# Kernel tuning notes

Measured on AMD Instinct MI355X. Metric: run time of the kernel, lower is better.

Reference implementation:

```python
import jax, jax.numpy as jnp
import numpy as np

ALPHA = 2000.0   # alpha (bandwidth penalty)
K = 8            # number of modes
MAX_N = 20       # max ADMM iterations; tol=0 -> loop always runs MAX_N-1 iters
DC = False


def setup_inputs() -> dict:
    key = jax.random.key(0)
    signal = jax.random.normal(key, (16, 8192), dtype=jnp.float32)  # (C, T)
    return {"signal": signal}


def _forward(signal):
    C, T = signal.shape
    F = 2 * T
    # mirror extension -> (C, 2T)
    f = jnp.concatenate([signal[:, :T // 2][:, ::-1], signal, signal[:, T // 2:][:, ::-1]], axis=1)
    t = jnp.linspace(1.0 / F, 1.0, F)
    freqs = (t - 0.5 - 1.0 / F).astype(jnp.float32)                  # (F,)
    # NOTE: torch.fft.fftshift with default dim shifts ALL dims (incl. channel dim);
    # jnp.fft.fftshift with axes=None matches this behavior exactly.
    f_hat = jnp.fft.fftshift(jnp.fft.fft(f))
    f_hat_plus = f_hat.at[:, :F // 2].set(0)                         # zero negative freqs
    fpos = f_hat_plus.T.astype(jnp.complex64)                        # (F, C)
    freqs_c = freqs.astype(jnp.complex64)
    fh = freqs[F // 2:]                                              # positive freqs (F/2,)
    alpha_c = jnp.complex64(ALPHA)

    omega0 = ((0.5 / K) * jnp.arange(K, dtype=jnp.float32)).astype(jnp.complex64)  # init == 1
    u0 = jnp.zeros((F, K, C), jnp.complex64)
    sum0 = jnp.zeros((F, C), jnp.complex64)

    def omega_update(u_k):                                           # u_k: (F, C)
        p = jnp.abs(u_k[F // 2:, :]) ** 2                            # (F/2, C)
        return (jnp.sum(fh @ p) / jnp.sum(p)).astype(jnp.complex64)

    def step(carry, _):
        u_prev, omega_prev, sum_uk = carry
        sum_uk = sum_uk + u_prev[:, K - 1, :] - u_prev[:, 0, :]
        us, omegas = [], []
        for k in range(K):                                           # sequential mode recurrence
            if k > 0:
                sum_uk = sum_uk + us[k - 1] - u_prev[:, k, :]
            # torch uses omega from the PREVIOUS outer iteration for all modes
            denom = 1.0 + alpha_c * jnp.square(freqs_c - omega_prev[k])   # (F,)
            u_k = (fpos - sum_uk) / denom[:, None]   # lamda_hat stays 0 (never updated in torch)
            us.append(u_k)
            if k == 0 and DC:
                omegas.append(jnp.complex64(0.0))
            else:
                omegas.append(omega_update(u_k))
        u_curr = jnp.stack(us, axis=1)                               # (F, K, C)
        omega_curr = jnp.stack(omegas)                               # (K,)
        return (u_curr, omega_curr, sum_uk), omega_curr

    (u_fin, _, _), omega_hist = jax.lax.scan(step, (u0, omega0, sum0), None, length=MAX_N - 1)
    omega = jnp.concatenate([omega0[None, :], omega_hist], axis=0)   # (MAX_N, K)

    # Hermitian completion of the half-spectrum (matches torch index assignments & order)
    pos = u_fin[F // 2:, :, :]                                       # (F/2, K, C)
    u_hat = jnp.zeros((F, K, C), jnp.complex64)
    u_hat = u_hat.at[F // 2:].set(pos)
    u_hat = u_hat.at[jnp.arange(F // 2, 0, -1)].set(jnp.conj(pos))   # overwrites bin F/2 w/ conj
    u_hat = u_hat.at[0].set(jnp.conj(u_hat[-1]))

    u_time = jnp.fft.ifft(jnp.fft.ifftshift(u_hat, axes=0), axis=0).real  # (F, K, C)
    u_c = jnp.transpose(u_time, (1, 0, 2)).astype(jnp.complex64)          # (K, F, C)
    u_c = u_c[:, F // 4:3 * F // 4, :]                                    # crop mirror -> (K, T, C)
    u_hat2 = jnp.conj(jnp.fft.fftshift(jnp.fft.fft(u_c, axis=1), axes=1)) # (K, T, C)
    u_hat2 = jnp.transpose(u_hat2, (1, 0, 2))                             # (T, K, C)
    # torch applies ifftshift with dim=-1, which is the CHANNEL dim here; replicate faithfully
    u_out = jnp.fft.ifftshift(u_c, axes=-1).real                          # (K, T, C)
    return u_out, u_hat2, omega


def reference(signal):
    return _forward(signal)
```

## Files before the change

### kernel.cpp

```cpp
#include <hip/hip_runtime.h>
#include <math.h>

#define NPAIR 131072
#define STEPS 19
#define VMD_BLOCKS 256
#define ND_BANKS 16

#define SW(a) ((a) ^ (((a) >> 5) & 31))

#define LD_RLX(p)    __hip_atomic_load((p),       __ATOMIC_RELAXED, __HIP_MEMORY_SCOPE_AGENT)
#define ST_RLX(p,v)  __hip_atomic_store((p),(v),  __ATOMIC_RELAXED, __HIP_MEMORY_SCOPE_AGENT)
#define FAA_RLX(p,v) __hip_atomic_fetch_add((p),(v),__ATOMIC_RELAXED, __HIP_MEMORY_SCOPE_AGENT)

#define D_NDB   0
#define D_CNT   4864
#define D_OHIST 5400

__device__ __forceinline__ float2 cadd(float2 a, float2 b){ return make_float2(a.x+b.x, a.y+b.y); }
__device__ __forceinline__ float2 csub(float2 a, float2 b){ return make_float2(a.x-b.x, a.y-b.y); }
__device__ __forceinline__ float2 cmul(float2 a, float2 b){
    return make_float2(a.x*b.x - a.y*b.y, a.x*b.y + a.y*b.x);
}
template<int SGN>
__device__ __forceinline__ float2 imul(float2 a){
    return (SGN > 0) ? make_float2(-a.y, a.x) : make_float2(a.y, -a.x);
}

template<int SGN>
__device__ __forceinline__ void dft8(const float2* a, float2* y){
    const float C = 0.70710678118654752f;
    const float sg = (SGN > 0) ? 1.f : -1.f;
    float2 t0 = cadd(a[0], a[4]), t1 = csub(a[0], a[4]);
    float2 t2 = cadd(a[2], a[6]), t3 = imul<SGN>(csub(a[2], a[6]));
    float2 E0 = cadd(t0, t2), E2 = csub(t0, t2), E1 = cadd(t1, t3), E3 = csub(t1, t3);
    float2 s0 = cadd(a[1], a[5]), s1 = csub(a[1], a[5]);
    float2 s2 = cadd(a[3], a[7]), s3 = imul<SGN>(csub(a[3], a[7]));
    float2 O0 = cadd(s0, s2), O2 = csub(s0, s2), O1 = cadd(s1, s3), O3 = csub(s1, s3);
    float2 w1 = make_float2(C, sg * C), w3 = make_float2(-C, sg * C);
    float2 R0 = O0, R1 = cmul(O1, w1), R2 = imul<SGN>(O2), R3 = cmul(O3, w3);
    y[0] = cadd(E0, R0); y[4] = csub(E0, R0);
    y[1] = cadd(E1, R1); y[5] = csub(E1, R1);
    y[2] = cadd(E2, R2); y[6] = csub(E2, R2);
    y[3] = cadd(E3, R3); y[7] = csub(E3, R3);
}

template<int SGN>
__device__ void lds_fft8192_r8(float2* lds, int tid){
    #pragma unroll
    for (int pi = 0; pi < 4; pi++){
        int ls = 3 * pi;
        int s  = 1 << ls;
        int nn = 8192 >> ls;
        int q = tid & (s - 1);
        float2 a[8], y[8];
        #pragma unroll
        for (int r = 0; r < 8; r++) a[r] = lds[SW(tid + (r << 10))];
        __syncthreads();
        dft8<SGN>(a, y);
        int p = tid >> ls;
        float ang = (float)(2 * p) / (float)nn;
        float sn, cs;
        sincospif(SGN > 0 ? ang : -ang, &sn, &cs);
        float2 w = make_float2(cs, sn);
        float2 wk = make_float2(1.f, 0.f);
        int o = q + ((tid - q) << 3);
        lds[SW(o)] = y[0];
        #pragma unroll
        for (int k = 1; k < 8; k++){
            wk = cmul(wk, w);
            lds[SW(o + (k << ls))] = cmul(y[k], wk);
        }
        __syncthreads();
    }
    #pragma unroll
    for (int w4 = 0; w4 < 4; w4++){
        int idx = (w4 << 10) + tid;
        float2 a = lds[SW(idx)], b = lds[SW(idx + 4096)];
        lds[SW(idx)]        = cadd(a, b);
        lds[SW(idx + 4096)] = csub(a, b);
    }
    __syncthreads();
}

template<int SGN>
__device__ void lds_fft4096_r8(float2* lds, int tid){
    #pragma unroll
    for (int pi = 0; pi < 4; pi++){
        int ls = 3 * pi;
        int s  = 1 << ls;
        int nn = 4096 >> ls;
        float2 a[8], y[8];
        int q = tid & (s - 1);
        if (tid < 512){
            #pragma unroll
            for (int r = 0; r < 8; r++) a[r] = lds[SW(tid + (r << 9))];
        }
        __syncthreads();
        if (tid < 512){
            dft8<SGN>(a, y);
            int p = tid >> ls;
            float ang = (float)(2 * p) / (float)nn;
            float sn, cs;
            sincospif(SGN > 0 ? ang : -ang, &sn, &cs);
            float2 w = make_float2(cs, sn);
            float2 wk = make_float2(1.f, 0.f);
            int o = q + ((tid - q) << 3);
            lds[SW(o)] = y[0];
            #pragma unroll
            for (int k = 1; k < 8; k++){
                wk = cmul(wk, w);
                lds[SW(o + (k << ls))] = cmul(y[k], wk);
            }
        }
        __syncthreads();
    }
}

__global__ __launch_bounds__(512) void k_stageA(const float* __restrict__ sig,
                                                float2* __restrict__ C,
                                                double* __restrict__ D){
    extern __shared__ float2 lds[];
    int tid = threadIdx.x;
    int bb  = blockIdx.x;
    int zi = bb * 512 + tid;
    if (zi < 5400) D[zi] = 0.0;
    int cw = bb >> 2, r4 = bb & 3;
    int cs = (cw + 8) & 15;
    const float* sp = sig + cs * 8192;
    #pragma unroll
    for (int i = 0; i < 8; i++){
        int p = i * 512 + tid;
        int x = 4 * p + r4;
        int mx = (x < 4096) ? (4095 - x) : ((x < 12288) ? (x - 4096) : (20479 - x));
        lds[SW(p)] = make_float2(sp[mx], 0.f);
    }
    __syncthreads();
    lds_fft4096_r8<-1>(lds, tid);
    float2* dst = C + (size_t)bb * 4096;
    #pragma unroll
    for (int i = 0; i < 8; i++){
        int j = i * 512 + tid;
        dst[j] = lds[SW(j)];
    }
}

__global__ __launch_bounds__(512, 2) void k_vmd_all(const float2* __restrict__ C,
                                                    float2* __restrict__ U,
                                                    double* __restrict__ D){
    double* NDB   = D + D_NDB;
    int*    CNT   = (int*)(D + D_CNT);
    double* OHIST = D + D_OHIST;

    int tid = blockIdx.x * 512 + threadIdx.x;
    int j = tid & 8191;
    int cw = tid >> 13;
    float fr = (float)j / 16384.0f;
    const float2* Cb = C + (size_t)(cw * 4) * 4096;
    int m = j & 4095;
    float2 C0 = Cb[m], C1 = Cb[4096 + m], C2 = Cb[8192 + m], C3 = Cb[12288 + m];
    float s1, c1, s2, c2;
    sincospif(-(float)j / 8192.0f, &s1, &c1);
    sincospif(-(float)j / 4096.0f, &s2, &c2);
    float2 w1 = make_float2(c1, s1), w2 = make_float2(c2, s2), w3 = cmul(w1, w2);
    float2 fv = cadd(cadd(C0, cmul(w1, C1)), cadd(cmul(w2, C2), cmul(w3, C3)));
    float fx = fv.x, fy = fv.y;
    float urx[8], ury[8], om[8];
    #pragma unroll
    for (int k = 0; k < 8; k++){ urx[k] = 0.f; ury[k] = 0.f; om[k] = 0.0625f * (float)k; }
    __shared__ float  lred[8][16];
    __shared__ double om_s[8];
    int lane = threadIdx.x & 63, wv = threadIdx.x >> 6;
    int mybank = (blockIdx.x & (ND_BANKS - 1)) * 16;
    int grp = blockIdx.x >> 4;

    for (int step = 0; step < STEPS; step++){
        if (step > 0){
            #pragma unroll
            for (int k = 0; k < 8; k++) om[k] = (float)om_s[k];
        }
        float sx = 0.f, sy = 0.f;
        #pragma unroll
        for (int k = 1; k < 8; k++){ sx += urx[k]; sy += ury[k]; }
        float lx = 0.f, ly = 0.f, nloc[8], dloc[8];
        #pragma unroll
        for (int k = 0; k < 8; k++){
            if (k > 0){ sx += lx - urx[k]; sy += ly - ury[k]; }
            float d = fr - om[k];
            float den = 1.0f + 2000.0f * d * d;
            float rden = 1.0f / den;
            float nx = (fx - sx) * rden, ny = (fy - sy) * rden;
            urx[k] = nx; ury[k] = ny;
            lx = nx; ly = ny;
            float pw = nx * nx + ny * ny;
            nloc[k] = fr * pw; dloc[k] = pw;
        }
        float s8[8];
        {
            bool hi = (lane & 32) != 0;
            #pragma unroll
            for (int k = 0; k < 8; k++){
                float t = hi ? nloc[k] : dloc[k];
                float r = __shfl_xor(t, 32);
                s8[k] = (hi ? dloc[k] : nloc[k]) + r;
            }
        }
        float s4v[4];
        {
            bool hi = (lane & 16) != 0;
            #pragma unroll
            for (int k = 0; k < 4; k++){
                float t = hi ? s8[k] : s8[k + 4];
                float r = __shfl_xor(t, 16);
                s4v[k] = (hi ? s8[k + 4] : s8[k]) + r;
            }
        }
        float s2v[2];
        {
            bool hi = (lane & 8) != 0;
            #pragma unroll
            for (int k = 0; k < 2; k++){
                float t = hi ? s4v[k] : s4v[k + 2];
                float r = __shfl_xor(t, 8);
                s2v[k] = (hi ? s4v[k + 2] : s4v[k]) + r;
            }
        }
        float sv;
        {
            bool hi = (lane & 4) != 0;
            float t = hi ? s2v[0] : s2v[1];
            float r = __shfl_xor(t, 4);
            sv = (hi ? s2v[1] : s2v[0]) + r;
        }
        sv += __shfl_xor(sv, 2);
        sv += __shfl_xor(sv, 1);
        if ((lane & 3) == 0) lred[wv][lane >> 2] = sv;
        __syncthreads();
        if (threadIdx.x < 16){
            double sum = 0.0;
            #pragma unroll
            for (int w = 0; w < 8; w++) sum += (double)lred[w][threadIdx.x];
            atomicAdd(&NDB[step * 256 + mybank + threadIdx.x], sum);
        }
        __syncthreads();
        if (step < STEPS - 1){
            if (threadIdx.x == 0){
                int target = 16 * (step + 1);
                int old = FAA_RLX(&CNT[grp * 32], 1);
                bool released = false;
                if (old == target - 1){
                    int rold = FAA_RLX(&CNT[512], 1);
                    if (rold == target - 1){
                        #pragma unroll
                        for (int g = 0; g < 16; g++)
                            ST_RLX(&CNT[576 + g * 32], step + 1);
                        released = true;
                    }
                }
                if (!released)
                    while (LD_RLX(&CNT[576 + grp * 32]) <= step) { }
            }
            __syncthreads();
            if (threadIdx.x < 8){
                const double* row = &NDB[step * 256];
                double n_ = 0.0, d_ = 0.0;
                #pragma unroll
                for (int bk = 0; bk < ND_BANKS; bk++){
                    n_ += LD_RLX(&row[bk * 16 + threadIdx.x]);
                    d_ += LD_RLX(&row[bk * 16 + 8 + threadIdx.x]);
                }
                double v = n_ / d_;
                om_s[threadIdx.x] = v;
                if (blockIdx.x == 0)
                    ST_RLX(&OHIST[step * 8 + threadIdx.x], v);
            }
            __syncthreads();
        }
    }
    #pragma unroll
    for (int k = 0; k < 8; k++) U[k * NPAIR + tid] = make_float2(urx[k], ury[k]);
}

__global__ __launch_bounds__(1024) void k_stageCD(float2* __restrict__ U){
    extern __shared__ float2 lds[];
    int tid = threadIdx.x;
    int b = blockIdx.x;
    const float2* pos = U + b * 8192;
    float* slice = (float*)(U) + (size_t)b * 16384;
    const float inv = 1.0f / 16384.0f;
    #pragma unroll
    for (int r = 0; r < 8; r++){
        int p = r * 1024 + tid;
        float2 Hk, HkM;
        if (p == 0){
            Hk  = make_float2(pos[0].x, 0.f);
            HkM = make_float2(pos[8191].x, 0.f);
        } else {
            Hk = pos[p];
            float2 q2 = pos[8192 - p];
            HkM = make_float2(q2.x, -q2.y);
        }
        float2 S  = cadd(Hk, HkM);
        float2 Dv = csub(Hk, HkM);
        float sn, cn;
        sincospif((float)p / 8192.0f, &sn, &cn);
        float2 c = cmul(make_float2(cn, sn), Dv);
        lds[SW(p)] = make_float2(S.x - c.y, S.y + c.x);
    }
    __syncthreads();
    lds_fft8192_r8<1>(lds, tid);
    float2 zreg[4];
    #pragma unroll
    for (int q = 2; q < 6; q++){
        int n = q * 1024 + tid;
        float2 z = lds[SW(n)];
        zreg[q - 2] = make_float2(z.x * inv, z.y * inv);
        *(float2*)&slice[2 * n - 4096] = zreg[q - 2];
    }
    __syncthreads();
    #pragma unroll
    for (int q = 0; q < 4; q++)
        lds[SW(q * 1024 + tid)] = zreg[q];
    __syncthreads();
    lds_fft4096_r8<-1>(lds, tid);
    #pragma unroll
    for (int q = 0; q < 4; q++){
        int k = q * 1024 + tid;
        float2 Wk = lds[SW(k)];
        float2 Wm = lds[SW((4096 - k) & 4095)];
        float ax = 0.5f * (Wk.x + Wm.x);
        float dx = Wk.x - Wm.x, dy = Wk.y + Wm.y;
        float bx = 0.5f * dy, by = -0.5f * dx;
        float sn, cn;
        sincospif(-(float)k / 4096.0f, &sn, &cn);
        float rey = ax + cn * bx - sn * by;
        slice[12288 + k] = rey;
        if (k > 0) slice[12288 - k] = rey;
        else       slice[8192]      = Wk.x - Wk.y;
    }
}

__global__ __launch_bounds__(256) void k_outs(const float* __restrict__ U32,
                                              const double* __restrict__ Dbase,
                                              float* __restrict__ out){
    __shared__ double smemd[128 * 65 / 2 + 140];
    float* smem = (float*)smemd;
    int bx = blockIdx.x;
    int tid = threadIdx.x;
    if (bx < 256){
        float (*tile)[257] = (float(*)[257])smem;
        int k  = bx >> 5;
        int t0 = (bx & 31) * 256;
        #pragma unroll
        for (int cw = 0; cw < 16; cw++)
            tile[cw][tid] = U32[((size_t)(k * 16 + cw)) * 16384 + t0 + tid];
        __syncthreads();
        #pragma unroll
        for (int i = 0; i < 16; i++){
            int flat = i * 256 + tid;
            int dt = flat >> 4, ch = flat & 15;
            int cw = (ch + 8) & 15;
            out[(size_t)k * 131072 + t0 * 16 + flat] = tile[cw][dt];
        }
    } else if (bx < 384){
        float (*tile)[65] = (float(*)[65])smem;
        int t0 = (bx - 256) * 64;
        #pragma unroll
        for (int i = 0; i < 32; i++){
            int flat = i * 256 + tid;
            int b = flat >> 6, dt = flat & 63;
            tile[b][dt] = U32[(size_t)b * 16384 + 8192 + t0 + dt];
        }
        __syncthreads();
        #pragma unroll
        for (int i = 0; i < 32; i++){
            int flat = i * 256 + tid;
            int dt = flat >> 7, b = flat & 127;
            out[1048576 + (size_t)(t0 + dt) * 128 + b] = tile[b][dt];
        }
    } else {
        const double* NDB   = Dbase + D_NDB;
        const double* OHIST = Dbase + D_OHIST;
        double* dsm = smemd;
        if (tid < 256) dsm[tid] = NDB[18 * 256 + tid];
        __syncthreads();
        if (tid < 8){
            double n_ = 0.0, d_ = 0.0;
            #pragma unroll
            for (int bk = 0; bk < ND_BANKS; bk++){
                n_ += dsm[bk * 16 + tid];
                d_ += dsm[bk * 16 + 8 + tid];
            }
            dsm[256 + tid] = n_ / d_;
        }
        __syncthreads();
        if (tid < 160){
            int row = tid >> 3, k = tid & 7;
            double v;
            if (row == 0)       v = 0.0625 * (double)k;
            else if (row <= 18) v = OHIST[(row - 1) * 8 + k];
            else                v = dsm[256 + k];
            out[2097152 + tid] = (float)v;
        }
    }
}

extern "C" void kernel_launch(void* const* d_in, const int* in_sizes, int n_in,
                              void* d_out, int out_size, void* d_ws, size_t ws_size,
                              hipStream_t stream){
    const float* sig = (const float*)d_in[0];
    float* out = (float*)d_out;
    char* p = (char*)d_ws;
    float2* U = (float2*)p;
    float2* C = (float2*)p;
    double* D = (double*)(p + (size_t)8 * 1024 * 1024);

    k_stageA<<<dim3(64), dim3(512), 32768, stream>>>(sig, C, D);
    k_vmd_all<<<dim3(VMD_BLOCKS), dim3(512), 0, stream>>>(C, U, D);
    k_stageCD<<<dim3(128), dim3(1024), 65536, stream>>>(U);
    k_outs<<<dim3(385), dim3(256), 0, stream>>>((const float*)U, D, out);
}
```

Baseline: 150.5 us.

## Fuse forward FFT stage into VMD kernel, recomputing sub-FFTs per block

The separate stage-A FFT kernel is removed. Each VMD block now computes the four 4096-point sub-FFTs for its channel in shared memory and keeps only the bins it needs in registers. This drops one kernel launch and the global round trip of the C buffer. In exchange, each channel's FFT work is repeated across 8 blocks, shared memory use grows to 32 KB per block, and the D buffer is now zeroed with a memset call instead of inside the kernel.

```diff
diff --git a/kernel.cpp b/kernel.cpp
--- a/kernel.cpp
+++ b/kernel.cpp
@@ -116,60 +116,51 @@
     }
 }
 
-__global__ __launch_bounds__(512) void k_stageA(const float* __restrict__ sig,
-                                                float2* __restrict__ C,
-                                                double* __restrict__ D){
-    extern __shared__ float2 lds[];
-    int tid = threadIdx.x;
-    int bb  = blockIdx.x;
-    int zi = bb * 512 + tid;
-    if (zi < 5400) D[zi] = 0.0;
-    int cw = bb >> 2, r4 = bb & 3;
-    int cs = (cw + 8) & 15;
-    const float* sp = sig + cs * 8192;
-    #pragma unroll
-    for (int i = 0; i < 8; i++){
-        int p = i * 512 + tid;
-        int x = 4 * p + r4;
-        int mx = (x < 4096) ? (4095 - x) : ((x < 12288) ? (x - 4096) : (20479 - x));
-        lds[SW(p)] = make_float2(sp[mx], 0.f);
-    }
-    __syncthreads();
-    lds_fft4096_r8<-1>(lds, tid);
-    float2* dst = C + (size_t)bb * 4096;
-    #pragma unroll
-    for (int i = 0; i < 8; i++){
-        int j = i * 512 + tid;
-        dst[j] = lds[SW(j)];
-    }
-}
-
-__global__ __launch_bounds__(512, 2) void k_vmd_all(const float2* __restrict__ C,
+__global__ __launch_bounds__(512, 2) void k_vmd_all(const float* __restrict__ sig,
                                                     float2* __restrict__ U,
                                                     double* __restrict__ D){
+    extern __shared__ float2 lds[];
     double* NDB   = D + D_NDB;
     int*    CNT   = (int*)(D + D_CNT);
     double* OHIST = D + D_OHIST;
 
-    int tid = blockIdx.x * 512 + threadIdx.x;
+    int t = threadIdx.x;
+    int tid = blockIdx.x * 512 + t;
     int j = tid & 8191;
     int cw = tid >> 13;
+    int m0 = (blockIdx.x & 7) * 512;
+    int cs = (cw + 8) & 15;
+    const float* sp = sig + cs * 8192;
+
+    float2 Creg[4];
+    for (int r4 = 0; r4 < 4; r4++){
+        #pragma unroll
+        for (int i = 0; i < 8; i++){
+            int p = i * 512 + t;
+            int x = 4 * p + r4;
+            int mx = (x < 4096) ? (4095 - x) : ((x < 12288) ? (x - 4096) : (20479 - x));
+            lds[SW(p)] = make_float2(sp[mx], 0.f);
+        }
+        __syncthreads();
+        lds_fft4096_r8<-1>(lds, t);
+        Creg[r4] = lds[SW(m0 + t)];
+        __syncthreads();
+    }
+
     float fr = (float)j / 16384.0f;
-    const float2* Cb = C + (size_t)(cw * 4) * 4096;
-    int m = j & 4095;
-    float2 C0 = Cb[m], C1 = Cb[4096 + m], C2 = Cb[8192 + m], C3 = Cb[12288 + m];
     float s1, c1, s2, c2;
     sincospif(-(float)j / 8192.0f, &s1, &c1);
     sincospif(-(float)j / 4096.0f, &s2, &c2);
     float2 w1 = make_float2(c1, s1), w2 = make_float2(c2, s2), w3 = cmul(w1, w2);
-    float2 fv = cadd(cadd(C0, cmul(w1, C1)), cadd(cmul(w2, C2), cmul(w3, C3)));
+    float2 fv = cadd(cadd(Creg[0], cmul(w1, Creg[1])),
+                     cadd(cmul(w2, Creg[2]), cmul(w3, Creg[3])));
     float fx = fv.x, fy = fv.y;
     float urx[8], ury[8], om[8];
     #pragma unroll
     for (int k = 0; k < 8; k++){ urx[k] = 0.f; ury[k] = 0.f; om[k] = 0.0625f * (float)k; }
     __shared__ float  lred[8][16];
     __shared__ double om_s[8];
-    int lane = threadIdx.x & 63, wv = threadIdx.x >> 6;
+    int lane = t & 63, wv = t >> 6;
     int mybank = (blockIdx.x & (ND_BANKS - 1)) * 16;
     int grp = blockIdx.x >> 4;
 
@@ -199,8 +190,8 @@
             bool hi = (lane & 32) != 0;
             #pragma unroll
             for (int k = 0; k < 8; k++){
-                float t = hi ? nloc[k] : dloc[k];
-                float r = __shfl_xor(t, 32);
+                float tt = hi ? nloc[k] : dloc[k];
+                float r = __shfl_xor(tt, 32);
                 s8[k] = (hi ? dloc[k] : nloc[k]) + r;
             }
         }
@@ -209,8 +200,8 @@
             bool hi = (lane & 16) != 0;
             #pragma unroll
             for (int k = 0; k < 4; k++){
-                float t = hi ? s8[k] : s8[k + 4];
-                float r = __shfl_xor(t, 16);
+                float tt = hi ? s8[k] : s8[k + 4];
+                float r = __shfl_xor(tt, 16);
                 s4v[k] = (hi ? s8[k + 4] : s8[k]) + r;
             }
         }
@@ -219,31 +210,31 @@
             bool hi = (lane & 8) != 0;
             #pragma unroll
             for (int k = 0; k < 2; k++){
-                float t = hi ? s4v[k] : s4v[k + 2];
-                float r = __shfl_xor(t, 8);
+                float tt = hi ? s4v[k] : s4v[k + 2];
+                float r = __shfl_xor(tt, 8);
                 s2v[k] = (hi ? s4v[k + 2] : s4v[k]) + r;
             }
         }
         float sv;
         {
             bool hi = (lane & 4) != 0;
-            float t = hi ? s2v[0] : s2v[1];
-            float r = __shfl_xor(t, 4);
+            float tt = hi ? s2v[0] : s2v[1];
+            float r = __shfl_xor(tt, 4);
             sv = (hi ? s2v[1] : s2v[0]) + r;
         }
         sv += __shfl_xor(sv, 2);
         sv += __shfl_xor(sv, 1);
         if ((lane & 3) == 0) lred[wv][lane >> 2] = sv;
         __syncthreads();
-        if (threadIdx.x < 16){
+        if (t < 16){
             double sum = 0.0;
             #pragma unroll
-            for (int w = 0; w < 8; w++) sum += (double)lred[w][threadIdx.x];
-            atomicAdd(&NDB[step * 256 + mybank + threadIdx.x], sum);
+            for (int w = 0; w < 8; w++) sum += (double)lred[w][t];
+            atomicAdd(&NDB[step * 256 + mybank + t], sum);
         }
         __syncthreads();
         if (step < STEPS - 1){
-            if (threadIdx.x == 0){
+            if (t == 0){
                 int target = 16 * (step + 1);
                 int old = FAA_RLX(&CNT[grp * 32], 1);
                 bool released = false;
@@ -260,18 +251,18 @@
                     while (LD_RLX(&CNT[576 + grp * 32]) <= step) { }
             }
             __syncthreads();
-            if (threadIdx.x < 8){
+            if (t < 8){
                 const double* row = &NDB[step * 256];
                 double n_ = 0.0, d_ = 0.0;
                 #pragma unroll
                 for (int bk = 0; bk < ND_BANKS; bk++){
-                    n_ += LD_RLX(&row[bk * 16 + threadIdx.x]);
-                    d_ += LD_RLX(&row[bk * 16 + 8 + threadIdx.x]);
+                    n_ += LD_RLX(&row[bk * 16 + t]);
+                    d_ += LD_RLX(&row[bk * 16 + 8 + t]);
                 }
                 double v = n_ / d_;
-                om_s[threadIdx.x] = v;
+                om_s[t] = v;
                 if (blockIdx.x == 0)
-                    ST_RLX(&OHIST[step * 8 + threadIdx.x], v);
+                    ST_RLX(&OHIST[step * 8 + t], v);
             }
             __syncthreads();
         }
@@ -411,11 +402,10 @@
     float* out = (float*)d_out;
     char* p = (char*)d_ws;
     float2* U = (float2*)p;
-    float2* C = (float2*)p;
     double* D = (double*)(p + (size_t)8 * 1024 * 1024);
 
-    k_stageA<<<dim3(64), dim3(512), 32768, stream>>>(sig, C, D);
-    k_vmd_all<<<dim3(VMD_BLOCKS), dim3(512), 0, stream>>>(C, U, D);
+    hipMemsetAsync(D, 0, 5400 * sizeof(double), stream);
+    k_vmd_all<<<dim3(VMD_BLOCKS), dim3(512), 32768, stream>>>(sig, U, D);
     k_stageCD<<<dim3(128), dim3(1024), 65536, stream>>>(U);
     k_outs<<<dim3(385), dim3(256), 0, stream>>>((const float*)U, D, out);
 }
```

New measurement: 163.7 us. +8.8%, slower.
